# Performance work log

Hardware: AMD Instinct MI355X
Metric: run time of the kernel (lower is better)

## Reference

```python
import jax, jax.numpy as jnp
from jax import lax
import numpy as np

WIN = 9
PAD = WIN // 2
DN = ('NCDHW', 'OIDHW', 'NCDHW')


def box_sum(x):
    """9x9x9 all-ones box sum (same padding), computed separably per axis.
    Matches the original dense depthwise conv3d with a ones kernel exactly in math."""
    C = x.shape[1]
    for axis in range(3):  # spatial axes D, H, W
        kshape = [1, 1, 1]
        kshape[axis] = WIN
        kernel = jnp.ones((C, 1, *kshape), dtype=x.dtype)
        padding = [(PAD, PAD) if i == axis else (0, 0) for i in range(3)]
        x = lax.conv_general_dilated(
            x, kernel, window_strides=(1, 1, 1), padding=padding,
            dimension_numbers=DN, feature_group_count=C)
    return x


def setup_inputs() -> dict:
    key = jax.random.key(0)
    k1, k2 = jax.random.split(key)
    shape = (2, 1, 160, 192, 160)
    y_true = jax.random.uniform(k1, shape, dtype=jnp.float32)
    y_pred = jax.random.uniform(k2, shape, dtype=jnp.float32)
    return {"y_true": y_true, "y_pred": y_pred}


def reference(y_true, y_pred):
    Ii, Ji = y_true, y_pred
    win_size = jnp.asarray(WIN ** 3, dtype=Ii.dtype)

    I_sum = box_sum(Ii)
    J_sum = box_sum(Ji)
    I2_sum = box_sum(Ii * Ii)
    J2_sum = box_sum(Ji * Ji)
    IJ_sum = box_sum(Ii * Ji)

    u_I = I_sum / win_size
    u_J = J_sum / win_size

    cross = IJ_sum - u_I * J_sum
    I_var = jnp.maximum(I2_sum - u_I * I_sum, 1e-05)
    J_var = jnp.maximum(J2_sum - u_J * J_sum, 1e-05)

    cc = cross * cross / (I_var * J_var + 1e-05)
    return -jnp.sum(cc)
```

## Files before the change

### kernel.cpp

```cpp
#include <hip/hip_runtime.h>
#include <hip/hip_fp16.h>

#define ND 2
#define DD 160
#define HH 192
#define WW 160
#define HW (HH * WW)
#define DHW (DD * HH * WW)

constexpr int TW  = 32;
constexpr int TH  = 16;
constexpr int HLO = TH + 8;
constexpr int FCH = 40;
constexpr int NCH = DD / FCH;
constexpr int NSL = FCH + 8;
constexpr int NR  = NSL / 2;

struct alignas(8) h4 { __half2 lo, hi; };

__device__ __forceinline__ void slide4(const float x[12], float S[4]) {
    float f = ((x[0] + x[1]) + (x[2] + x[3]))
            + ((x[4] + x[5]) + (x[6] + x[7])) + x[8];
    S[0] = f;
    f += x[9]  - x[0]; S[1] = f;
    f += x[10] - x[1]; S[2] = f;
    f += x[11] - x[2]; S[3] = f;
}

__global__ __launch_bounds__(512, 4)
void ncc_fused2(const float* __restrict__ I, const float* __restrict__ J,
                float* __restrict__ outp)
{
    __shared__ float4 sws[2][HLO][TW + 1];
    __shared__ float  sw4[2][HLO][TW + 1];
    __shared__ h4     ring4[9][512];
    __shared__ __half ring1[9][512];
    __shared__ float  wred[8];

    const int tid = threadIdx.x;
    const int w0  = blockIdx.x * TW;
    const int h0  = blockIdx.y * TH;
    const int z   = blockIdx.z;
    const int n   = z >> 2;
    const int d0  = (z & 3) * FCH;

    const bool ajob = (tid < 384);
    const int  sl   = tid / 192;
    const int  rj   = tid - sl * 192;
    const int  arow = rj >> 3;
    const int  awg  = rj & 7;
    const int  agh  = h0 + arow - 4;
    const bool ahok = (agh >= 0) && (agh < HH);
    const int  agws = w0 + awg * 4 - 4;

    const int oh = tid >> 5;
    const int ow = tid & 31;
    const int h  = h0 + oh, w = w0 + ow;
    const float cW  = (float)(min(w + 4, WW - 1) - max(w - 4, 0) + 1);
    const float cH  = (float)(min(h + 4, HH - 1) - max(h - 4, 0) + 1);
    const float cHW = cW * cH;

    {
        h4 zz; zz.lo = __floats2half2_rn(0.f, 0.f); zz.hi = zz.lo;
        const __half z1 = __float2half(0.f);
        #pragma unroll
        for (int q = 0; q < 9; ++q) { ring4[q][tid] = zz; ring1[q][tid] = z1; }
    }

    float run0 = 0.f, run1 = 0.f, run2 = 0.f, run3 = 0.f, run4 = 0.f;
    float acc = 0.f;
    const float inv = 1.0f / 729.0f;

    #pragma unroll 1
    for (int g = 0; g < 3; ++g) {
        #pragma unroll
        for (int r = 0; r < 9; ++r) {
            const int rr = g * 9 + r;
            if (rr < NR) {
                const int s0  = 2 * rr;
                const int dd0 = d0 - 4 + s0;
                if (ajob) {
                    const int dd = dd0 + sl;
                    if (dd >= 0 && dd < DD) {
                        const int rbase = (n * DD + dd) * HW + agh * WW;
                        float a[12], b[12];
                        #pragma unroll
                        for (int c = 0; c < 3; ++c) {
                            const int gw = agws + 4 * c;
                            float4 va = make_float4(0.f, 0.f, 0.f, 0.f), vb = va;
                            if (ahok && gw >= 0 && gw < WW) {
                                va = *(const float4*)(I + rbase + gw);
                                vb = *(const float4*)(J + rbase + gw);
                                va.x -= 0.5f; va.y -= 0.5f; va.z -= 0.5f; va.w -= 0.5f;
                                vb.x -= 0.5f; vb.y -= 0.5f; vb.z -= 0.5f; vb.w -= 0.5f;
                            }
                            *(float4*)&a[4 * c] = va;
                            *(float4*)&b[4 * c] = vb;
                        }
                        float S0[4], S1[4], S2[4], S3[4], S4[4], f[12];
                        slide4(a, S0);
                        slide4(b, S1);
                        #pragma unroll
                        for (int i = 0; i < 12; ++i) f[i] = a[i] * a[i];
                        slide4(f, S2);
                        #pragma unroll
                        for (int i = 0; i < 12; ++i) f[i] = b[i] * b[i];
                        slide4(f, S3);
                        #pragma unroll
                        for (int i = 0; i < 12; ++i) f[i] = a[i] * b[i];
                        slide4(f, S4);
                        #pragma unroll
                        for (int t = 0; t < 4; ++t) {
                            sws[sl][arow][awg * 4 + t] =
                                make_float4(S0[t], S1[t], S2[t], S3[t]);
                            sw4[sl][arow][awg * 4 + t] = S4[t];
                        }
                    }
                }
                __syncthreads();
                #pragma unroll
                for (int half = 0; half < 2; ++half) {
                    const int s   = s0 + half;
                    const int ddx = dd0 + half;
                    float t0 = 0.f, t1 = 0.f, t2 = 0.f, t3 = 0.f, t4 = 0.f;
                    if (ddx >= 0 && ddx < DD) {
                        #pragma unroll
                        for (int q = 0; q < 9; ++q) {
                            const float4 v = sws[half][oh + q][ow];
                            t0 += v.x; t1 += v.y; t2 += v.z; t3 += v.w;
                            t4 += sw4[half][oh + q][ow];
                        }
                    }
                    h4 nh;
                    nh.lo = __floats2half2_rn(t0, t1);
                    nh.hi = __floats2half2_rn(t2, t3);
                    const __half n4 = __float2half(t4);
                    const int jj = (2 * r + half) % 9;
                    const h4     po = ring4[jj][tid];
                    const __half p4 = ring1[jj][tid];
                    run0 += __half2float(nh.lo.x) - __half2float(po.lo.x);
                    run1 += __half2float(nh.lo.y) - __half2float(po.lo.y);
                    run2 += __half2float(nh.hi.x) - __half2float(po.hi.x);
                    run3 += __half2float(nh.hi.y) - __half2float(po.hi.y);
                    run4 += __half2float(n4)      - __half2float(p4);
                    ring4[jj][tid] = nh;
                    ring1[jj][tid] = n4;
                    if (s >= 8) {
                        const int d = d0 + s - 8;
                        const float cD  = (float)(min(d + 4, DD - 1) - max(d - 4, 0) + 1);
                        const float cnt = cHW * cD;
                        const float Is = run0 + 0.5f * cnt;
                        const float Js = run1 + 0.5f * cnt;
                        const float I2 = run2 + run0 + 0.25f * cnt;
                        const float J2 = run3 + run1 + 0.25f * cnt;
                        const float IJ = run4 + 0.5f * (run0 + run1) + 0.25f * cnt;
                        const float uI = Is * inv, uJ = Js * inv;
                        const float cross = IJ - uI * Js;
                        const float Iv = fmaxf(I2 - uI * Is, 1e-5f);
                        const float Jv = fmaxf(J2 - uJ * Js, 1e-5f);
                        acc += cross * cross / (Iv * Jv + 1e-5f);
                    }
                }
                __syncthreads();
            }
        }
    }

    #pragma unroll
    for (int off = 32; off > 0; off >>= 1)
        acc += __shfl_down(acc, off, 64);
    const int lane = tid & 63, wid = tid >> 6;
    if (lane == 0) wred[wid] = acc;
    __syncthreads();
    if (tid == 0) {
        float s = 0.f;
        #pragma unroll
        for (int i = 0; i < 8; ++i) s += wred[i];
        atomicAdd(outp, -s);
    }
}

extern "C" void kernel_launch(void* const* d_in, const int* in_sizes, int n_in,
                              void* d_out, int out_size, void* d_ws, size_t ws_size,
                              hipStream_t stream)
{
    const float* I = (const float*)d_in[0];
    const float* J = (const float*)d_in[1];
    float* out = (float*)d_out;

    hipMemsetAsync(out, 0, sizeof(float), stream);
    dim3 grid(WW / TW, HH / TH, ND * NCH);
    ncc_fused2<<<grid, 512, 0, stream>>>(I, J, out);
}
```

Measured before the change: 166.4 us.

## Specialize warps into loader and H-sum roles with sliding H window and prefetch

Threads 0-383 now only load and compute W-direction sums, and they prefetch the next slab pair into registers before the barrier. Threads 384-511 (two wavefronts) handle the H-direction sum, each covering four output rows with a sliding window instead of 9-tap sums per row. The goal is to hide global load latency and cut redundant LDS reads in the H pass. The cost is that the whole H and D pass plus the epilogue now runs on only 128 threads, which risks a serial bottleneck and higher register pressure. The min-waves launch bound was also dropped.

```diff
diff --git a/kernel.cpp b/kernel.cpp
--- a/kernel.cpp
+++ b/kernel.cpp
@@ -27,8 +27,8 @@
     f += x[11] - x[2]; S[3] = f;
 }
 
-__global__ __launch_bounds__(512, 4)
-void ncc_fused2(const float* __restrict__ I, const float* __restrict__ J,
+__global__ __launch_bounds__(512)
+void ncc_fused3(const float* __restrict__ I, const float* __restrict__ J,
                 float* __restrict__ outp)
 {
     __shared__ float4 sws[2][HLO][TW + 1];
@@ -53,12 +53,19 @@
     const bool ahok = (agh >= 0) && (agh < HH);
     const int  agws = w0 + awg * 4 - 4;
 
-    const int oh = tid >> 5;
-    const int ow = tid & 31;
-    const int h  = h0 + oh, w = w0 + ow;
-    const float cW  = (float)(min(w + 4, WW - 1) - max(w - 4, 0) + 1);
-    const float cH  = (float)(min(h + 4, HH - 1) - max(h - 4, 0) + 1);
-    const float cHW = cW * cH;
+    const bool bjob = (tid >= 384);
+    const int  tid2 = tid - 384;
+    const int  hq   = (tid2 >> 5) * 4;
+    const int  ow   = tid2 & 31;
+    float cHW[4];
+    #pragma unroll
+    for (int k = 0; k < 4; ++k) {
+        const int hg = h0 + hq + k, wg = w0 + ow;
+        const float cWv = (float)(min(wg + 4, WW - 1) - max(wg - 4, 0) + 1);
+        const float cHv = (float)(min(hg + 4, HH - 1) - max(hg - 4, 0) + 1);
+        cHW[k] = cWv * cHv;
+    }
+    const int colbase = hq * 32 + ow;
 
     {
         h4 zz; zz.lo = __floats2half2_rn(0.f, 0.f); zz.hi = zz.lo;
@@ -66,10 +73,36 @@
         #pragma unroll
         for (int q = 0; q < 9; ++q) { ring4[q][tid] = zz; ring1[q][tid] = z1; }
     }
-
-    float run0 = 0.f, run1 = 0.f, run2 = 0.f, run3 = 0.f, run4 = 0.f;
+    __syncthreads();
+
+    float run[4][5];
+    #pragma unroll
+    for (int k = 0; k < 4; ++k)
+        #pragma unroll
+        for (int p = 0; p < 5; ++p) run[k][p] = 0.f;
     float acc = 0.f;
     const float inv = 1.0f / 729.0f;
+
+    float pa[12], pb[12];
+    auto load_ab = [&](int rrt) {
+        const int dd  = d0 - 4 + 2 * rrt + sl;
+        const bool dok = (dd >= 0) && (dd < DD);
+        const int rbase = (n * DD + dd) * HW + agh * WW;
+        #pragma unroll
+        for (int c = 0; c < 3; ++c) {
+            const int gw = agws + 4 * c;
+            float4 va = make_float4(0.f, 0.f, 0.f, 0.f), vb = va;
+            if (dok && ahok && gw >= 0 && gw < WW) {
+                va = *(const float4*)(I + rbase + gw);
+                vb = *(const float4*)(J + rbase + gw);
+                va.x -= 0.5f; va.y -= 0.5f; va.z -= 0.5f; va.w -= 0.5f;
+                vb.x -= 0.5f; vb.y -= 0.5f; vb.z -= 0.5f; vb.w -= 0.5f;
+            }
+            *(float4*)&pa[4 * c] = va;
+            *(float4*)&pb[4 * c] = vb;
+        }
+    };
+    if (ajob) load_ab(0);
 
     #pragma unroll 1
     for (int g = 0; g < 3; ++g) {
@@ -82,32 +115,17 @@
                 if (ajob) {
                     const int dd = dd0 + sl;
                     if (dd >= 0 && dd < DD) {
-                        const int rbase = (n * DD + dd) * HW + agh * WW;
-                        float a[12], b[12];
-                        #pragma unroll
-                        for (int c = 0; c < 3; ++c) {
-                            const int gw = agws + 4 * c;
-                            float4 va = make_float4(0.f, 0.f, 0.f, 0.f), vb = va;
-                            if (ahok && gw >= 0 && gw < WW) {
-                                va = *(const float4*)(I + rbase + gw);
-                                vb = *(const float4*)(J + rbase + gw);
-                                va.x -= 0.5f; va.y -= 0.5f; va.z -= 0.5f; va.w -= 0.5f;
-                                vb.x -= 0.5f; vb.y -= 0.5f; vb.z -= 0.5f; vb.w -= 0.5f;
-                            }
-                            *(float4*)&a[4 * c] = va;
-                            *(float4*)&b[4 * c] = vb;
-                        }
                         float S0[4], S1[4], S2[4], S3[4], S4[4], f[12];
-                        slide4(a, S0);
-                        slide4(b, S1);
-                        #pragma unroll
-                        for (int i = 0; i < 12; ++i) f[i] = a[i] * a[i];
+                        slide4(pa, S0);
+                        slide4(pb, S1);
+                        #pragma unroll
+                        for (int i = 0; i < 12; ++i) f[i] = pa[i] * pa[i];
                         slide4(f, S2);
                         #pragma unroll
-                        for (int i = 0; i < 12; ++i) f[i] = b[i] * b[i];
+                        for (int i = 0; i < 12; ++i) f[i] = pb[i] * pb[i];
                         slide4(f, S3);
                         #pragma unroll
-                        for (int i = 0; i < 12; ++i) f[i] = a[i] * b[i];
+                        for (int i = 0; i < 12; ++i) f[i] = pa[i] * pb[i];
                         slide4(f, S4);
                         #pragma unroll
                         for (int t = 0; t < 4; ++t) {
@@ -116,49 +134,102 @@
                             sw4[sl][arow][awg * 4 + t] = S4[t];
                         }
                     }
+                    if (rr + 1 < NR) load_ab(rr + 1);
                 }
                 __syncthreads();
-                #pragma unroll
-                for (int half = 0; half < 2; ++half) {
-                    const int s   = s0 + half;
-                    const int ddx = dd0 + half;
-                    float t0 = 0.f, t1 = 0.f, t2 = 0.f, t3 = 0.f, t4 = 0.f;
-                    if (ddx >= 0 && ddx < DD) {
-                        #pragma unroll
-                        for (int q = 0; q < 9; ++q) {
-                            const float4 v = sws[half][oh + q][ow];
-                            t0 += v.x; t1 += v.y; t2 += v.z; t3 += v.w;
-                            t4 += sw4[half][oh + q][ow];
+                if (bjob) {
+                    #pragma unroll
+                    for (int half = 0; half < 2; ++half) {
+                        const int s   = s0 + half;
+                        const int ddx = dd0 + half;
+                        float t0=0.f,t1=0.f,t2=0.f,t3=0.f,t4=0.f;
+                        float u0=0.f,u1=0.f,u2=0.f,u3=0.f,u4=0.f;
+                        float v0=0.f,v1=0.f,v2=0.f,v3=0.f,v4=0.f;
+                        float x0=0.f,x1=0.f,x2=0.f,x3=0.f,x4=0.f;
+                        if (ddx >= 0 && ddx < DD) {
+                            float a0x,a0y,a0z,a0w,a04;
+                            float a1x,a1y,a1z,a1w,a14;
+                            float a2x,a2y,a2z,a2w,a24;
+                            {
+                                const float4 v = sws[half][hq][ow];
+                                a0x=v.x; a0y=v.y; a0z=v.z; a0w=v.w;
+                                a04 = sw4[half][hq][ow];
+                                t0=a0x; t1=a0y; t2=a0z; t3=a0w; t4=a04;
+                            }
+                            {
+                                const float4 v = sws[half][hq+1][ow];
+                                a1x=v.x; a1y=v.y; a1z=v.z; a1w=v.w;
+                                a14 = sw4[half][hq+1][ow];
+                                t0+=a1x; t1+=a1y; t2+=a1z; t3+=a1w; t4+=a14;
+                            }
+                            {
+                                const float4 v = sws[half][hq+2][ow];
+                                a2x=v.x; a2y=v.y; a2z=v.z; a2w=v.w;
+                                a24 = sw4[half][hq+2][ow];
+                                t0+=a2x; t1+=a2y; t2+=a2z; t3+=a2w; t4+=a24;
+                            }
+                            #pragma unroll
+                            for (int q = 3; q < 9; ++q) {
+                                const float4 v = sws[half][hq+q][ow];
+                                t0+=v.x; t1+=v.y; t2+=v.z; t3+=v.w;
+                                t4+=sw4[half][hq+q][ow];
+                            }
+                            {
+                                const float4 v = sws[half][hq+9][ow];
+                                u0=t0+v.x-a0x; u1=t1+v.y-a0y; u2=t2+v.z-a0z;
+                                u3=t3+v.w-a0w; u4=t4+sw4[half][hq+9][ow]-a04;
+                            }
+                            {
+                                const float4 v = sws[half][hq+10][ow];
+                                v0=u0+v.x-a1x; v1=u1+v.y-a1y; v2=u2+v.z-a1z;
+                                v3=u3+v.w-a1w; v4=u4+sw4[half][hq+10][ow]-a14;
+                            }
+                            {
+                                const float4 v = sws[half][hq+11][ow];
+                                x0=v0+v.x-a2x; x1=v1+v.y-a2y; x2=v2+v.z-a2z;
+                                x3=v3+v.w-a2w; x4=v4+sw4[half][hq+11][ow]-a24;
+                            }
                         }
-                    }
-                    h4 nh;
-                    nh.lo = __floats2half2_rn(t0, t1);
-                    nh.hi = __floats2half2_rn(t2, t3);
-                    const __half n4 = __float2half(t4);
-                    const int jj = (2 * r + half) % 9;
-                    const h4     po = ring4[jj][tid];
-                    const __half p4 = ring1[jj][tid];
-                    run0 += __half2float(nh.lo.x) - __half2float(po.lo.x);
-                    run1 += __half2float(nh.lo.y) - __half2float(po.lo.y);
-                    run2 += __half2float(nh.hi.x) - __half2float(po.hi.x);
-                    run3 += __half2float(nh.hi.y) - __half2float(po.hi.y);
-                    run4 += __half2float(n4)      - __half2float(p4);
-                    ring4[jj][tid] = nh;
-                    ring1[jj][tid] = n4;
-                    if (s >= 8) {
-                        const int d = d0 + s - 8;
-                        const float cD  = (float)(min(d + 4, DD - 1) - max(d - 4, 0) + 1);
-                        const float cnt = cHW * cD;
-                        const float Is = run0 + 0.5f * cnt;
-                        const float Js = run1 + 0.5f * cnt;
-                        const float I2 = run2 + run0 + 0.25f * cnt;
-                        const float J2 = run3 + run1 + 0.25f * cnt;
-                        const float IJ = run4 + 0.5f * (run0 + run1) + 0.25f * cnt;
-                        const float uI = Is * inv, uJ = Js * inv;
-                        const float cross = IJ - uI * Js;
-                        const float Iv = fmaxf(I2 - uI * Is, 1e-5f);
-                        const float Jv = fmaxf(J2 - uJ * Js, 1e-5f);
-                        acc += cross * cross / (Iv * Jv + 1e-5f);
+                        const int jj = (2 * r + half) % 9;
+                        const float cD =
+                            (float)(min((d0 + s - 8) + 4, DD - 1) -
+                                    max((d0 + s - 8) - 4, 0) + 1);
+                        #define DO_OUT(K, B0, B1, B2, B3, B4)                  \
+                        {                                                      \
+                            const int col = colbase + 32 * (K);                \
+                            h4 nh;                                             \
+                            nh.lo = __floats2half2_rn(B0, B1);                 \
+                            nh.hi = __floats2half2_rn(B2, B3);                 \
+                            const __half n4h = __float2half(B4);               \
+                            const h4     po = ring4[jj][col];                  \
+                            const __half p4 = ring1[jj][col];                  \
+                            run[K][0] += __half2float(nh.lo.x) - __half2float(po.lo.x); \
+                            run[K][1] += __half2float(nh.lo.y) - __half2float(po.lo.y); \
+                            run[K][2] += __half2float(nh.hi.x) - __half2float(po.hi.x); \
+                            run[K][3] += __half2float(nh.hi.y) - __half2float(po.hi.y); \
+                            run[K][4] += __half2float(n4h)     - __half2float(p4);      \
+                            ring4[jj][col] = nh;                               \
+                            ring1[jj][col] = n4h;                              \
+                            if (s >= 8) {                                      \
+                                const float cnt = cHW[K] * cD;                 \
+                                const float Is = run[K][0] + 0.5f * cnt;       \
+                                const float Js = run[K][1] + 0.5f * cnt;       \
+                                const float I2 = run[K][2] + run[K][0] + 0.25f * cnt; \
+                                const float J2 = run[K][3] + run[K][1] + 0.25f * cnt; \
+                                const float IJ = run[K][4] +                   \
+                                    0.5f * (run[K][0] + run[K][1]) + 0.25f * cnt; \
+                                const float uI = Is * inv, uJ = Js * inv;      \
+                                const float cross = IJ - uI * Js;              \
+                                const float Iv = fmaxf(I2 - uI * Is, 1e-5f);   \
+                                const float Jv = fmaxf(J2 - uJ * Js, 1e-5f);   \
+                                acc += cross * cross / (Iv * Jv + 1e-5f);      \
+                            }                                                  \
+                        }
+                        DO_OUT(0, t0, t1, t2, t3, t4)
+                        DO_OUT(1, u0, u1, u2, u3, u4)
+                        DO_OUT(2, v0, v1, v2, v3, v4)
+                        DO_OUT(3, x0, x1, x2, x3, x4)
+                        #undef DO_OUT
                     }
                 }
                 __syncthreads();
@@ -173,10 +244,10 @@
     if (lane == 0) wred[wid] = acc;
     __syncthreads();
     if (tid == 0) {
-        float s = 0.f;
-        #pragma unroll
-        for (int i = 0; i < 8; ++i) s += wred[i];
-        atomicAdd(outp, -s);
+        float ssum = 0.f;
+        #pragma unroll
+        for (int i = 0; i < 8; ++i) ssum += wred[i];
+        atomicAdd(outp, -ssum);
     }
 }
 
@@ -190,5 +261,5 @@
 
     hipMemsetAsync(out, 0, sizeof(float), stream);
     dim3 grid(WW / TW, HH / TH, ND * NCH);
-    ncc_fused2<<<grid, 512, 0, stream>>>(I, J, out);
+    ncc_fused3<<<grid, 512, 0, stream>>>(I, J, out);
 }
```

After: 258.1 us. 1.55x slower.

## Prefetch next slab into registers and store W-sums as half in LDS

Applied to the files above, without the earlier changes.

Global loads of I and J for the next pair of depth slices are issued right after computing the current one, so they overlap with the barrier and the H-direction reduction. The W-direction partial sums are packed as half precision into a 16-byte LDS entry instead of float4 plus a separate float, and the H sum is accumulated with packed half adds. The launch-bounds occupancy hint is dropped. The prefetch adds register pressure, and the half accumulation over 9 rows loses precision compared with float.

```diff
diff --git a/kernel.cpp b/kernel.cpp
--- a/kernel.cpp
+++ b/kernel.cpp
@@ -16,7 +16,8 @@
 constexpr int NSL = FCH + 8;
 constexpr int NR  = NSL / 2;
 
-struct alignas(8) h4 { __half2 lo, hi; };
+struct alignas(8)  h4 { __half2 lo, hi; };
+struct alignas(16) h8 { __half2 a, b, c, d; };
 
 __device__ __forceinline__ void slide4(const float x[12], float S[4]) {
     float f = ((x[0] + x[1]) + (x[2] + x[3]))
@@ -27,12 +28,11 @@
     f += x[11] - x[2]; S[3] = f;
 }
 
-__global__ __launch_bounds__(512, 4)
-void ncc_fused2(const float* __restrict__ I, const float* __restrict__ J,
+__global__ __launch_bounds__(512)
+void ncc_fused4(const float* __restrict__ I, const float* __restrict__ J,
                 float* __restrict__ outp)
 {
-    __shared__ float4 sws[2][HLO][TW + 1];
-    __shared__ float  sw4[2][HLO][TW + 1];
+    __shared__ h8     sws[2][HLO][TW + 1];
     __shared__ h4     ring4[9][512];
     __shared__ __half ring1[9][512];
     __shared__ float  wred[8];
@@ -71,6 +71,27 @@
     float acc = 0.f;
     const float inv = 1.0f / 729.0f;
 
+    float pa[12], pb[12];
+    auto load_ab = [&](int rrt) {
+        const int dd  = d0 - 4 + 2 * rrt + sl;
+        const bool dok = (dd >= 0) && (dd < DD);
+        const int rbase = (n * DD + dd) * HW + agh * WW;
+        #pragma unroll
+        for (int c = 0; c < 3; ++c) {
+            const int gw = agws + 4 * c;
+            float4 va = make_float4(0.f, 0.f, 0.f, 0.f), vb = va;
+            if (dok && ahok && gw >= 0 && gw < WW) {
+                va = *(const float4*)(I + rbase + gw);
+                vb = *(const float4*)(J + rbase + gw);
+                va.x -= 0.5f; va.y -= 0.5f; va.z -= 0.5f; va.w -= 0.5f;
+                vb.x -= 0.5f; vb.y -= 0.5f; vb.z -= 0.5f; vb.w -= 0.5f;
+            }
+            *(float4*)&pa[4 * c] = va;
+            *(float4*)&pb[4 * c] = vb;
+        }
+    };
+    if (ajob) load_ab(0);
+
     #pragma unroll 1
     for (int g = 0; g < 3; ++g) {
         #pragma unroll
@@ -82,69 +103,58 @@
                 if (ajob) {
                     const int dd = dd0 + sl;
                     if (dd >= 0 && dd < DD) {
-                        const int rbase = (n * DD + dd) * HW + agh * WW;
-                        float a[12], b[12];
-                        #pragma unroll
-                        for (int c = 0; c < 3; ++c) {
-                            const int gw = agws + 4 * c;
-                            float4 va = make_float4(0.f, 0.f, 0.f, 0.f), vb = va;
-                            if (ahok && gw >= 0 && gw < WW) {
-                                va = *(const float4*)(I + rbase + gw);
-                                vb = *(const float4*)(J + rbase + gw);
-                                va.x -= 0.5f; va.y -= 0.5f; va.z -= 0.5f; va.w -= 0.5f;
-                                vb.x -= 0.5f; vb.y -= 0.5f; vb.z -= 0.5f; vb.w -= 0.5f;
-                            }
-                            *(float4*)&a[4 * c] = va;
-                            *(float4*)&b[4 * c] = vb;
-                        }
                         float S0[4], S1[4], S2[4], S3[4], S4[4], f[12];
-                        slide4(a, S0);
-                        slide4(b, S1);
-                        #pragma unroll
-                        for (int i = 0; i < 12; ++i) f[i] = a[i] * a[i];
+                        slide4(pa, S0);
+                        slide4(pb, S1);
+                        #pragma unroll
+                        for (int i = 0; i < 12; ++i) f[i] = pa[i] * pa[i];
                         slide4(f, S2);
                         #pragma unroll
-                        for (int i = 0; i < 12; ++i) f[i] = b[i] * b[i];
+                        for (int i = 0; i < 12; ++i) f[i] = pb[i] * pb[i];
                         slide4(f, S3);
                         #pragma unroll
-                        for (int i = 0; i < 12; ++i) f[i] = a[i] * b[i];
+                        for (int i = 0; i < 12; ++i) f[i] = pa[i] * pb[i];
                         slide4(f, S4);
                         #pragma unroll
                         for (int t = 0; t < 4; ++t) {
-                            sws[sl][arow][awg * 4 + t] =
-                                make_float4(S0[t], S1[t], S2[t], S3[t]);
-                            sw4[sl][arow][awg * 4 + t] = S4[t];
+                            h8 e;
+                            e.a = __floats2half2_rn(S0[t], S1[t]);
+                            e.b = __floats2half2_rn(S2[t], S3[t]);
+                            e.c = __floats2half2_rn(S4[t], 0.f);
+                            e.d = __floats2half2_rn(0.f, 0.f);
+                            sws[sl][arow][awg * 4 + t] = e;
                         }
                     }
+                    if (rr + 1 < NR) load_ab(rr + 1);
                 }
                 __syncthreads();
                 #pragma unroll
                 for (int half = 0; half < 2; ++half) {
                     const int s   = s0 + half;
                     const int ddx = dd0 + half;
-                    float t0 = 0.f, t1 = 0.f, t2 = 0.f, t3 = 0.f, t4 = 0.f;
+                    __half2 a01 = __floats2half2_rn(0.f, 0.f);
+                    __half2 a23 = a01, a4 = a01;
                     if (ddx >= 0 && ddx < DD) {
                         #pragma unroll
                         for (int q = 0; q < 9; ++q) {
-                            const float4 v = sws[half][oh + q][ow];
-                            t0 += v.x; t1 += v.y; t2 += v.z; t3 += v.w;
-                            t4 += sw4[half][oh + q][ow];
+                            const h8 v = sws[half][oh + q][ow];
+                            a01 = __hadd2(a01, v.a);
+                            a23 = __hadd2(a23, v.b);
+                            a4  = __hadd2(a4,  v.c);
                         }
                     }
-                    h4 nh;
-                    nh.lo = __floats2half2_rn(t0, t1);
-                    nh.hi = __floats2half2_rn(t2, t3);
-                    const __half n4 = __float2half(t4);
+                    h4 nh; nh.lo = a01; nh.hi = a23;
+                    const __half n4h = __low2half(a4);
                     const int jj = (2 * r + half) % 9;
                     const h4     po = ring4[jj][tid];
                     const __half p4 = ring1[jj][tid];
-                    run0 += __half2float(nh.lo.x) - __half2float(po.lo.x);
-                    run1 += __half2float(nh.lo.y) - __half2float(po.lo.y);
-                    run2 += __half2float(nh.hi.x) - __half2float(po.hi.x);
-                    run3 += __half2float(nh.hi.y) - __half2float(po.hi.y);
-                    run4 += __half2float(n4)      - __half2float(p4);
+                    run0 += __low2float(nh.lo)  - __low2float(po.lo);
+                    run1 += __high2float(nh.lo) - __high2float(po.lo);
+                    run2 += __low2float(nh.hi)  - __low2float(po.hi);
+                    run3 += __high2float(nh.hi) - __high2float(po.hi);
+                    run4 += __half2float(n4h)   - __half2float(p4);
                     ring4[jj][tid] = nh;
-                    ring1[jj][tid] = n4;
+                    ring1[jj][tid] = n4h;
                     if (s >= 8) {
                         const int d = d0 + s - 8;
                         const float cD  = (float)(min(d + 4, DD - 1) - max(d - 4, 0) + 1);
@@ -173,10 +183,10 @@
     if (lane == 0) wred[wid] = acc;
     __syncthreads();
     if (tid == 0) {
-        float s = 0.f;
-        #pragma unroll
-        for (int i = 0; i < 8; ++i) s += wred[i];
-        atomicAdd(outp, -s);
+        float ssum = 0.f;
+        #pragma unroll
+        for (int i = 0; i < 8; ++i) ssum += wred[i];
+        atomicAdd(outp, -ssum);
     }
 }
 
@@ -190,5 +200,5 @@
 
     hipMemsetAsync(out, 0, sizeof(float), stream);
     dim3 grid(WW / TW, HH / TH, ND * NCH);
-    ncc_fused2<<<grid, 512, 0, stream>>>(I, J, out);
+    ncc_fused4<<<grid, 512, 0, stream>>>(I, J, out);
 }
```

Result: slower. 184.3 us (+10.7%).

## Prefetch depth slices via async global-to-LDS loads and hold ring slots in registers

Applied to the files above, without the earlier changes.

Replaces the direct global float4 loads of I and J with __builtin_amdgcn_global_load_lds into a double-slot shared staging buffer. The next pair of depth slices is issued right after the first barrier so the loads overlap the H-direction reduction and ring update. Four of the nine depth-ring slots move from LDS into registers, which shrinks shared memory but adds branchy register selection. The launch_bounds minimum-occupancy hint is dropped. The staging layout relies on each wave's 16-byte-per-lane LDS placement lining up with the arow*40 indexing, which is fragile.

```diff
diff --git a/kernel.cpp b/kernel.cpp
--- a/kernel.cpp
+++ b/kernel.cpp
@@ -27,14 +27,15 @@
     f += x[11] - x[2]; S[3] = f;
 }
 
-__global__ __launch_bounds__(512, 4)
-void ncc_fused2(const float* __restrict__ I, const float* __restrict__ J,
+__global__ __launch_bounds__(512)
+void ncc_fused6(const float* __restrict__ I, const float* __restrict__ J,
                 float* __restrict__ outp)
 {
+    __shared__ float  sraw[2][2048];
     __shared__ float4 sws[2][HLO][TW + 1];
     __shared__ float  sw4[2][HLO][TW + 1];
-    __shared__ h4     ring4[9][512];
-    __shared__ __half ring1[9][512];
+    __shared__ h4     ring4[5][512];
+    __shared__ __half ring1[5][512];
     __shared__ float  wred[8];
 
     const int tid = threadIdx.x;
@@ -60,16 +61,45 @@
     const float cH  = (float)(min(h + 4, HH - 1) - max(h - 4, 0) + 1);
     const float cHW = cW * cH;
 
+    const bool chI   = tid < 240;
+    const bool chPad = tid >= 480;
+    const int  cr    = chI ? tid : (tid - 240);
+    const int  crow  = cr / 10, cwc = cr - crow * 10;
+    const int  cgh   = h0 + crow - 4;
+    const int  cgw   = w0 - 4 + cwc * 4;
+    const bool spok  = !chPad && cgh >= 0 && cgh < HH && cgw >= 0 && cgw < WW;
+    const float* fptr = chI ? I : J;
+    const int  spoff = spok ? (cgh * WW + cgw) : 0;
+    const int  ldsbase = (tid & ~63) * 4;
+
+    auto stage = [&](int p, int dd) {
+        const bool dok = (dd >= 0) && (dd < DD);
+        const float* src = (dok && spok)
+            ? (fptr + (size_t)(n * DD + dd) * HW + spoff)
+            : fptr;
+        __builtin_amdgcn_global_load_lds(
+            (const __attribute__((address_space(1))) void*)src,
+            (__attribute__((address_space(3))) void*)&sraw[p][ldsbase],
+            16, 0, 0);
+    };
+
+    h4 rg5, rg6, rg7, rg8; __half rs5, rs6, rs7, rs8;
     {
         h4 zz; zz.lo = __floats2half2_rn(0.f, 0.f); zz.hi = zz.lo;
         const __half z1 = __float2half(0.f);
         #pragma unroll
-        for (int q = 0; q < 9; ++q) { ring4[q][tid] = zz; ring1[q][tid] = z1; }
+        for (int q = 0; q < 5; ++q) { ring4[q][tid] = zz; ring1[q][tid] = z1; }
+        rg5 = rg6 = rg7 = rg8 = zz;
+        rs5 = rs6 = rs7 = rs8 = z1;
     }
 
     float run0 = 0.f, run1 = 0.f, run2 = 0.f, run3 = 0.f, run4 = 0.f;
     float acc = 0.f;
     const float inv = 1.0f / 729.0f;
+
+    stage(0, d0 - 4 + 0);
+    stage(1, d0 - 4 + 1);
+    __syncthreads();
 
     #pragma unroll 1
     for (int g = 0; g < 3; ++g) {
@@ -81,22 +111,24 @@
                 const int dd0 = d0 - 4 + s0;
                 if (ajob) {
                     const int dd = dd0 + sl;
-                    if (dd >= 0 && dd < DD) {
-                        const int rbase = (n * DD + dd) * HW + agh * WW;
-                        float a[12], b[12];
-                        #pragma unroll
-                        for (int c = 0; c < 3; ++c) {
-                            const int gw = agws + 4 * c;
-                            float4 va = make_float4(0.f, 0.f, 0.f, 0.f), vb = va;
-                            if (ahok && gw >= 0 && gw < WW) {
-                                va = *(const float4*)(I + rbase + gw);
-                                vb = *(const float4*)(J + rbase + gw);
-                                va.x -= 0.5f; va.y -= 0.5f; va.z -= 0.5f; va.w -= 0.5f;
-                                vb.x -= 0.5f; vb.y -= 0.5f; vb.z -= 0.5f; vb.w -= 0.5f;
-                            }
-                            *(float4*)&a[4 * c] = va;
-                            *(float4*)&b[4 * c] = vb;
+                    const bool dok = (dd >= 0) && (dd < DD);
+                    float a[12], b[12];
+                    const int fi = arow * 40 + awg * 4;
+                    #pragma unroll
+                    for (int c = 0; c < 3; ++c) {
+                        const int gw = agws + 4 * c;
+                        float4 va = *(const float4*)&sraw[sl][fi + 4 * c];
+                        float4 vb = *(const float4*)&sraw[sl][960 + fi + 4 * c];
+                        if (dok && ahok && gw >= 0 && gw < WW) {
+                            va.x -= 0.5f; va.y -= 0.5f; va.z -= 0.5f; va.w -= 0.5f;
+                            vb.x -= 0.5f; vb.y -= 0.5f; vb.z -= 0.5f; vb.w -= 0.5f;
+                        } else {
+                            va = make_float4(0.f, 0.f, 0.f, 0.f); vb = va;
                         }
+                        *(float4*)&a[4 * c] = va;
+                        *(float4*)&b[4 * c] = vb;
+                    }
+                    if (dok) {
                         float S0[4], S1[4], S2[4], S3[4], S4[4], f[12];
                         slide4(a, S0);
                         slide4(b, S1);
@@ -118,6 +150,10 @@
                     }
                 }
                 __syncthreads();
+                if (rr + 1 < NR) {
+                    stage(0, dd0 + 2);
+                    stage(1, dd0 + 3);
+                }
                 #pragma unroll
                 for (int half = 0; half < 2; ++half) {
                     const int s   = s0 + half;
@@ -134,17 +170,24 @@
                     h4 nh;
                     nh.lo = __floats2half2_rn(t0, t1);
                     nh.hi = __floats2half2_rn(t2, t3);
-                    const __half n4 = __float2half(t4);
+                    const __half n4h = __float2half(t4);
                     const int jj = (2 * r + half) % 9;
-                    const h4     po = ring4[jj][tid];
-                    const __half p4 = ring1[jj][tid];
-                    run0 += __half2float(nh.lo.x) - __half2float(po.lo.x);
-                    run1 += __half2float(nh.lo.y) - __half2float(po.lo.y);
-                    run2 += __half2float(nh.hi.x) - __half2float(po.hi.x);
-                    run3 += __half2float(nh.hi.y) - __half2float(po.hi.y);
-                    run4 += __half2float(n4)      - __half2float(p4);
-                    ring4[jj][tid] = nh;
-                    ring1[jj][tid] = n4;
+                    h4 po; __half p4;
+                    if (jj < 5)       { po = ring4[jj][tid]; p4 = ring1[jj][tid]; }
+                    else if (jj == 5) { po = rg5; p4 = rs5; }
+                    else if (jj == 6) { po = rg6; p4 = rs6; }
+                    else if (jj == 7) { po = rg7; p4 = rs7; }
+                    else              { po = rg8; p4 = rs8; }
+                    run0 += __low2float(nh.lo)  - __low2float(po.lo);
+                    run1 += __high2float(nh.lo) - __high2float(po.lo);
+                    run2 += __low2float(nh.hi)  - __low2float(po.hi);
+                    run3 += __high2float(nh.hi) - __high2float(po.hi);
+                    run4 += __half2float(n4h)   - __half2float(p4);
+                    if (jj < 5)       { ring4[jj][tid] = nh; ring1[jj][tid] = n4h; }
+                    else if (jj == 5) { rg5 = nh; rs5 = n4h; }
+                    else if (jj == 6) { rg6 = nh; rs6 = n4h; }
+                    else if (jj == 7) { rg7 = nh; rs7 = n4h; }
+                    else              { rg8 = nh; rs8 = n4h; }
                     if (s >= 8) {
                         const int d = d0 + s - 8;
                         const float cD  = (float)(min(d + 4, DD - 1) - max(d - 4, 0) + 1);
@@ -173,10 +216,10 @@
     if (lane == 0) wred[wid] = acc;
     __syncthreads();
     if (tid == 0) {
-        float s = 0.f;
+        float ssum = 0.f;
         #pragma unroll
-        for (int i = 0; i < 8; ++i) s += wred[i];
-        atomicAdd(outp, -s);
+        for (int i = 0; i < 8; ++i) ssum += wred[i];
+        atomicAdd(outp, -ssum);
     }
 }
 
@@ -190,5 +233,5 @@
 
     hipMemsetAsync(out, 0, sizeof(float), stream);
     dim3 grid(WW / TW, HH / TH, ND * NCH);
-    ncc_fused2<<<grid, 512, 0, stream>>>(I, J, out);
+    ncc_fused6<<<grid, 512, 0, stream>>>(I, J, out);
 }
```

New measurement: 158.6 us. -4.7%, faster.
